# Kernel optimization log

Hardware: AMD Instinct MI355X
Metric: run time of the kernel (lower is better)

Reference implementation:

```python
import jax, jax.numpy as jnp
import numpy as np

B, D, L, H = 2048, 64, 64, 512  # batch, in_dim, latent_space, hidden


def setup_inputs() -> dict:
    key = jax.random.key(0)
    ks = jax.random.split(key, 12)
    inp = {
        "x": jax.random.normal(ks[0], (B, D), jnp.float32),
        "koopman": jax.random.normal(ks[1], (B, L, D), jnp.float32),
    }
    dims = [(L, H), (H, H), (H, H), (H, D)]
    k = 2
    for pfx in ("s", "t"):
        for j, (fi, fo) in enumerate(dims):
            inp[f"{pfx}W{j+1}"] = jax.random.normal(ks[k], (fi, fo), jnp.float32) / np.sqrt(fi).astype(np.float32)
            inp[f"{pfx}b{j+1}"] = jnp.zeros((fo,), jnp.float32)
            k += 1
    return inp


def _mlp(z, W1, b1, W2, b2, W3, b3, W4, b4):
    h = jnp.tanh(z @ W1 + b1)
    h = jnp.tanh(h @ W2 + b2)
    h = jnp.tanh(h @ W3 + b3)
    return h @ W4 + b4


def reference(x, koopman,
              sW1, sb1, sW2, sb2, sW3, sb3, sW4, sb4,
              tW1, tb1, tW2, tb2, tW3, tb3, tW4, tb4):
    # koopman: (B, L, D) -> z: (B, D, L); column i of the torch loop is z[:, i, :]
    z = jnp.swapaxes(koopman, 1, 2)
    s = _mlp(z, sW1, sb1, sW2, sb2, sW3, sb3, sW4, sb4)  # (B, D, D)
    t = _mlp(z, tW1, tb1, tW2, tb2, tW3, tb3, tW4, tb4)  # (B, D, D)
    # loop kept only output column i for input column i -> diagonal over last two dims
    ds = jnp.diagonal(s, axis1=1, axis2=2)  # (B, D)
    dt = jnp.diagonal(t, axis1=1, axis2=2)  # (B, D)
    return (x - dt) * jnp.exp(-ds)
```

## Files before the change

### kernel.cpp

```cpp
#include <hip/hip_runtime.h>


typedef _Float16 f16;
typedef _Float16 f16x8 __attribute__((ext_vector_type(8)));
typedef float f32x4 __attribute__((ext_vector_type(4)));

#define WPACK_PER_NET 589824
#define OFF_W1 0
#define OFF_W2 32768
#define OFF_W3 294912
#define OFF_W4T 557056
#define WPACK_BYTES (2u * WPACK_PER_NET * sizeof(f16))

__global__ void pack_weights(const float* __restrict__ sW1, const float* __restrict__ sW2,
                             const float* __restrict__ sW3, const float* __restrict__ sW4,
                             const float* __restrict__ tW1, const float* __restrict__ tW2,
                             const float* __restrict__ tW3, const float* __restrict__ tW4,
                             f16* __restrict__ dst) {
  int idx8 = (blockIdx.x * 256 + threadIdx.x) * 8;
  if (idx8 >= 2 * WPACK_PER_NET) return;
  int net = idx8 >= WPACK_PER_NET;
  int f = idx8 - net * WPACK_PER_NET;
  const float* W1 = net ? tW1 : sW1;
  const float* W2 = net ? tW2 : sW2;
  const float* W3 = net ? tW3 : sW3;
  const float* W4 = net ? tW4 : sW4;
  f16x8 o;
  if (f < OFF_W2) {
    int lane = (f >> 3) & 63, nt = (f >> 9) & 31, kk = f >> 14;
    int r0 = kk * 32 + (lane >> 4) * 8, c = nt * 16 + (lane & 15);
#pragma unroll
    for (int j = 0; j < 8; j++) o[j] = (f16)W1[(r0 + j) * 512 + c];
  } else if (f < OFF_W3) {
    int f2 = f - OFF_W2;
    int lane = (f2 >> 3) & 63, nt = (f2 >> 9) & 31, kk = f2 >> 14;
    int r0 = kk * 32 + (lane >> 4) * 8, c = nt * 16 + (lane & 15);
#pragma unroll
    for (int j = 0; j < 8; j++) o[j] = (f16)W2[(r0 + j) * 512 + c];
  } else if (f < OFF_W4T) {
    int f3 = f - OFF_W3;
    int lane = (f3 >> 3) & 63, nt = (f3 >> 9) & 31, kk = f3 >> 14;
    int r0 = kk * 32 + (lane >> 4) * 8, c = nt * 16 + (lane & 15);
#pragma unroll
    for (int j = 0; j < 8; j++) o[j] = (f16)W3[(r0 + j) * 512 + c];
  } else {
    int f4 = f - OFF_W4T;
    int i = f4 >> 9, k0 = f4 & 511;
#pragma unroll
    for (int j = 0; j < 8; j++) o[j] = (f16)W4[(k0 + j) * 64 + i];
  }
  *(f16x8*)(dst + net * WPACK_PER_NET + f) = o;
}

__device__ __forceinline__ int aidx(int m, int k) {
  return (((k >> 5) * 4 + (m >> 4)) * 64 + (m & 15) + ((k >> 3) & 3) * 16) * 8 + (k & 7);
}

__device__ __forceinline__ float fast_tanh(float x) {
  float e = __expf(x + x);
  return fmaf(-2.0f, __builtin_amdgcn_rcpf(e + 1.0f), 1.0f);
}

template <bool PACKED>
__device__ __forceinline__ void load_b(const f16* __restrict__ Wblk,
                                       const float* __restrict__ Wraw,
                                       int kk, int wave, int lane, f16x8* bdst) {
  if (PACKED) {
#pragma unroll
    for (int nt = 0; nt < 2; nt++)
      bdst[nt] = *(const f16x8*)(Wblk + kk * 16384 + ((wave * 2 + nt) * 64 + lane) * 8);
  } else {
    int n0 = wave * 32 + (lane & 15);
    int kb = kk * 32 + (lane >> 4) * 8;
#pragma unroll
    for (int nt = 0; nt < 2; nt++) {
      f16x8 v;
#pragma unroll
      for (int j = 0; j < 8; j++) v[j] = (f16)Wraw[(kb + j) * 512 + n0 + nt * 16];
      bdst[nt] = v;
    }
  }
}

template <int NS, bool PACKED>
__device__ __forceinline__ void mlp_layer(const f16* __restrict__ Wblk,
                                          const float* __restrict__ Wraw,
                                          const float* __restrict__ bias,
                                          const f16* Asrc, f16* Hout,
                                          int wave, int lane, int sbase) {
  f32x4 acc[4][2];
#pragma unroll
  for (int nt = 0; nt < 2; nt++) {
    float bv = bias[wave * 32 + nt * 16 + (lane & 15)];
#pragma unroll
    for (int mt = 0; mt < 4; mt++) acc[mt][nt] = f32x4{bv, bv, bv, bv};
  }

  f16x8 bb[2][2];
  load_b<PACKED>(Wblk, Wraw, 0, wave, lane, bb[0]);
#pragma unroll
  for (int kk = 0; kk < NS; kk++) {
    if (kk + 1 < NS) load_b<PACKED>(Wblk, Wraw, kk + 1, wave, lane, bb[(kk + 1) & 1]);
    const f16* ab = Asrc + kk * 2048 + lane * 8;
    f16x8 a[4];
#pragma unroll
    for (int mt = 0; mt < 4; mt++) a[mt] = *(const f16x8*)(ab + mt * 512);
#pragma unroll
    for (int mt = 0; mt < 4; mt++)
#pragma unroll
      for (int nt = 0; nt < 2; nt++)
        acc[mt][nt] = __builtin_amdgcn_mfma_f32_16x16x32_f16(a[mt], bb[kk & 1][nt],
                                                             acc[mt][nt], 0, 0, 0);
  }
  __syncthreads();

  f16* hb = Hout + sbase;
#pragma unroll
  for (int mt = 0; mt < 4; mt++)
#pragma unroll
    for (int nt = 0; nt < 2; nt++)
#pragma unroll
      for (int r = 0; r < 4; r++)
        hb[mt * 512 + nt * 256 + r * 8] = (f16)fast_tanh(acc[mt][nt][r]);
  __syncthreads();
}

template <bool PACKED>
__global__ __launch_bounds__(1024, 4) void decoder_main(
    const float* __restrict__ x, const float* __restrict__ koop,
    const f16* __restrict__ wpack,
    const float* __restrict__ sW1, const float* __restrict__ sW2,
    const float* __restrict__ sW3, const float* __restrict__ sW4,
    const float* __restrict__ tW1, const float* __restrict__ tW2,
    const float* __restrict__ tW3, const float* __restrict__ tW4,
    const float* __restrict__ sb1, const float* __restrict__ sb2,
    const float* __restrict__ sb3, const float* __restrict__ sb4,
    const float* __restrict__ tb1, const float* __restrict__ tb2,
    const float* __restrict__ tb3, const float* __restrict__ tb4,
    float* __restrict__ out) {
  __shared__ __align__(16) f16 ZA[4096];
  __shared__ __align__(16) f16 HA[32768];
  __shared__ float redBuf[2][64];

  const int b = blockIdx.x;
  const int t = threadIdx.x;
  const int wave = t >> 6, lane = t & 63;
  const int sbase =
      wave * 2048 + (lane >> 4) * 32 + ((lane & 15) >> 3) * 128 + (lane & 7);

  const float* kb = koop + b * 4096;
#pragma unroll
  for (int i = 0; i < 4; i++) {
    int flat = t + 1024 * i;
    ZA[aidx(flat & 63, flat >> 6)] = (f16)kb[flat];
  }
  __syncthreads();

  for (int net = 0; net < 2; net++) {
    const f16* wb = PACKED ? (wpack + net * WPACK_PER_NET) : (const f16*)0;
    const float* W1 = net ? tW1 : sW1;
    const float* W2 = net ? tW2 : sW2;
    const float* W3 = net ? tW3 : sW3;
    const float* W4 = net ? tW4 : sW4;
    const float* b1 = net ? tb1 : sb1;
    const float* b2 = net ? tb2 : sb2;
    const float* b3 = net ? tb3 : sb3;
    const float* b4 = net ? tb4 : sb4;
    mlp_layer<2, PACKED>(PACKED ? wb + OFF_W1 : 0, W1, b1, ZA, HA, wave, lane, sbase);
    mlp_layer<16, PACKED>(PACKED ? wb + OFF_W2 : 0, W2, b2, HA, HA, wave, lane, sbase);
    mlp_layer<16, PACKED>(PACKED ? wb + OFF_W3 : 0, W3, b3, HA, HA, wave, lane, sbase);

    int i = t >> 4, sub = t & 15;
    float p = 0.f;
#pragma unroll
    for (int q = 0; q < 4; q++) {
      int k0 = sub * 32 + q * 8;
      f16x8 hv = *(const f16x8*)&HA[aidx(i, k0)];
      if (PACKED) {
        f16x8 wv = *(const f16x8*)&wb[OFF_W4T + i * 512 + k0];
#pragma unroll
        for (int j = 0; j < 8; j++) p += (float)hv[j] * (float)wv[j];
      } else {
#pragma unroll
        for (int j = 0; j < 8; j++) p += (float)hv[j] * W4[(k0 + j) * 64 + i];
      }
    }
    p += __shfl_down(p, 8, 16);
    p += __shfl_down(p, 4, 16);
    p += __shfl_down(p, 2, 16);
    p += __shfl_down(p, 1, 16);
    if (sub == 0) redBuf[net][i] = p + b4[i];
    __syncthreads();
  }

  if (t < 64) {
    out[b * 64 + t] = (x[b * 64 + t] - redBuf[1][t]) * __expf(-redBuf[0][t]);
  }
}

extern "C" void kernel_launch(void* const* d_in, const int* in_sizes, int n_in,
                              void* d_out, int out_size, void* d_ws, size_t ws_size,
                              hipStream_t stream) {
  const float* x    = (const float*)d_in[0];
  const float* koop = (const float*)d_in[1];
  const float* sW1 = (const float*)d_in[2];  const float* sb1 = (const float*)d_in[3];
  const float* sW2 = (const float*)d_in[4];  const float* sb2 = (const float*)d_in[5];
  const float* sW3 = (const float*)d_in[6];  const float* sb3 = (const float*)d_in[7];
  const float* sW4 = (const float*)d_in[8];  const float* sb4 = (const float*)d_in[9];
  const float* tW1 = (const float*)d_in[10]; const float* tb1 = (const float*)d_in[11];
  const float* tW2 = (const float*)d_in[12]; const float* tb2 = (const float*)d_in[13];
  const float* tW3 = (const float*)d_in[14]; const float* tb3 = (const float*)d_in[15];
  const float* tW4 = (const float*)d_in[16]; const float* tb4 = (const float*)d_in[17];
  float* out = (float*)d_out;

  if (ws_size >= (size_t)WPACK_BYTES) {
    f16* wpack = (f16*)d_ws;
    pack_weights<<<576, 256, 0, stream>>>(sW1, sW2, sW3, sW4, tW1, tW2, tW3, tW4, wpack);
    decoder_main<true><<<2048, 1024, 0, stream>>>(
        x, koop, wpack, sW1, sW2, sW3, sW4, tW1, tW2, tW3, tW4,
        sb1, sb2, sb3, sb4, tb1, tb2, tb3, tb4, out);
  } else {
    decoder_main<false><<<2048, 1024, 0, stream>>>(
        x, koop, (const f16*)0, sW1, sW2, sW3, sW4, tW1, tW2, tW3, tW4,
        sb1, sb2, sb3, sb4, tb1, tb2, tb3, tb4, out);
  }
}
```

Before: 436.3 us.

## Split each batch row across two 512-thread blocks with wider per-wave N tiles

Each block now handles 32 of the 64 latent columns for one batch row, launching twice as many blocks with half the threads and half the shared memory. Waves compute a 2x4 MFMA tile (64 output columns) instead of 4x2, so fewer A fragments are reused across more B loads. Tanh is evaluated into registers before the barrier so it overlaps other waves. The cost is that every block streams the full weight set, doubling total weight reads from L2.

Result: slower. 494.7 us (+13.4%).

```diff
diff --git a/kernel.cpp b/kernel.cpp
--- a/kernel.cpp
+++ b/kernel.cpp
@@ -52,8 +52,8 @@
   *(f16x8*)(dst + net * WPACK_PER_NET + f) = o;
 }
 
-__device__ __forceinline__ int aidx(int m, int k) {
-  return (((k >> 5) * 4 + (m >> 4)) * 64 + (m & 15) + ((k >> 3) & 3) * 16) * 8 + (k & 7);
+__device__ __forceinline__ int aidx32(int m, int k) {
+  return (((k >> 5) * 2 + (m >> 4)) * 64 + (m & 15) + ((k >> 3) & 3) * 16) * 8 + (k & 7);
 }
 
 __device__ __forceinline__ float fast_tanh(float x) {
@@ -67,13 +67,13 @@
                                        int kk, int wave, int lane, f16x8* bdst) {
   if (PACKED) {
 #pragma unroll
-    for (int nt = 0; nt < 2; nt++)
-      bdst[nt] = *(const f16x8*)(Wblk + kk * 16384 + ((wave * 2 + nt) * 64 + lane) * 8);
+    for (int nt = 0; nt < 4; nt++)
+      bdst[nt] = *(const f16x8*)(Wblk + kk * 16384 + ((wave * 4 + nt) * 64 + lane) * 8);
   } else {
-    int n0 = wave * 32 + (lane & 15);
+    int n0 = wave * 64 + (lane & 15);
     int kb = kk * 32 + (lane >> 4) * 8;
 #pragma unroll
-    for (int nt = 0; nt < 2; nt++) {
+    for (int nt = 0; nt < 4; nt++) {
       f16x8 v;
 #pragma unroll
       for (int j = 0; j < 8; j++) v[j] = (f16)Wraw[(kb + j) * 512 + n0 + nt * 16];
@@ -88,45 +88,56 @@
                                           const float* __restrict__ bias,
                                           const f16* Asrc, f16* Hout,
                                           int wave, int lane, int sbase) {
-  f32x4 acc[4][2];
-#pragma unroll
-  for (int nt = 0; nt < 2; nt++) {
-    float bv = bias[wave * 32 + nt * 16 + (lane & 15)];
-#pragma unroll
-    for (int mt = 0; mt < 4; mt++) acc[mt][nt] = f32x4{bv, bv, bv, bv};
-  }
-
-  f16x8 bb[2][2];
+  f32x4 acc[2][4];
+#pragma unroll
+  for (int nt = 0; nt < 4; nt++) {
+    float bv = bias[wave * 64 + nt * 16 + (lane & 15)];
+#pragma unroll
+    for (int mt = 0; mt < 2; mt++) acc[mt][nt] = f32x4{bv, bv, bv, bv};
+  }
+
+  f16x8 bb[2][4];
   load_b<PACKED>(Wblk, Wraw, 0, wave, lane, bb[0]);
 #pragma unroll
   for (int kk = 0; kk < NS; kk++) {
     if (kk + 1 < NS) load_b<PACKED>(Wblk, Wraw, kk + 1, wave, lane, bb[(kk + 1) & 1]);
-    const f16* ab = Asrc + kk * 2048 + lane * 8;
-    f16x8 a[4];
-#pragma unroll
-    for (int mt = 0; mt < 4; mt++) a[mt] = *(const f16x8*)(ab + mt * 512);
-#pragma unroll
-    for (int mt = 0; mt < 4; mt++)
-#pragma unroll
-      for (int nt = 0; nt < 2; nt++)
+    const f16* ab = Asrc + kk * 1024 + lane * 8;
+    f16x8 a[2];
+#pragma unroll
+    for (int mt = 0; mt < 2; mt++) a[mt] = *(const f16x8*)(ab + mt * 512);
+#pragma unroll
+    for (int mt = 0; mt < 2; mt++)
+#pragma unroll
+      for (int nt = 0; nt < 4; nt++)
         acc[mt][nt] = __builtin_amdgcn_mfma_f32_16x16x32_f16(a[mt], bb[kk & 1][nt],
                                                              acc[mt][nt], 0, 0, 0);
   }
+
+  f16 hreg[32];
+#pragma unroll
+  for (int mt = 0; mt < 2; mt++)
+#pragma unroll
+    for (int nt = 0; nt < 4; nt++)
+#pragma unroll
+      for (int r = 0; r < 4; r++)
+        hreg[(mt * 4 + nt) * 4 + r] = (f16)fast_tanh(acc[mt][nt][r]);
+
   __syncthreads();
 
   f16* hb = Hout + sbase;
 #pragma unroll
-  for (int mt = 0; mt < 4; mt++)
-#pragma unroll
-    for (int nt = 0; nt < 2; nt++)
+  for (int mt = 0; mt < 2; mt++)
+#pragma unroll
+    for (int nt = 0; nt < 4; nt++)
 #pragma unroll
       for (int r = 0; r < 4; r++)
-        hb[mt * 512 + nt * 256 + r * 8] = (f16)fast_tanh(acc[mt][nt][r]);
+        hb[(nt >> 1) * 1024 + (nt & 1) * 256 + mt * 512 + r * 8] =
+            hreg[(mt * 4 + nt) * 4 + r];
   __syncthreads();
 }
 
 template <bool PACKED>
-__global__ __launch_bounds__(1024, 4) void decoder_main(
+__global__ __launch_bounds__(512, 4) void decoder_main(
     const float* __restrict__ x, const float* __restrict__ koop,
     const f16* __restrict__ wpack,
     const float* __restrict__ sW1, const float* __restrict__ sW2,
@@ -138,21 +149,23 @@
     const float* __restrict__ tb1, const float* __restrict__ tb2,
     const float* __restrict__ tb3, const float* __restrict__ tb4,
     float* __restrict__ out) {
-  __shared__ __align__(16) f16 ZA[4096];
-  __shared__ __align__(16) f16 HA[32768];
-  __shared__ float redBuf[2][64];
-
-  const int b = blockIdx.x;
+  __shared__ __align__(16) f16 ZA[2048];
+  __shared__ __align__(16) f16 HA[16384];
+  __shared__ float redBuf[2][32];
+
+  const int bid = blockIdx.x;
+  const int b = bid >> 1, rr = bid & 1;
   const int t = threadIdx.x;
   const int wave = t >> 6, lane = t & 63;
   const int sbase =
       wave * 2048 + (lane >> 4) * 32 + ((lane & 15) >> 3) * 128 + (lane & 7);
 
-  const float* kb = koop + b * 4096;
+  const float* kb = koop + b * 4096 + rr * 32;
 #pragma unroll
   for (int i = 0; i < 4; i++) {
-    int flat = t + 1024 * i;
-    ZA[aidx(flat & 63, flat >> 6)] = (f16)kb[flat];
+    int flat = t + 512 * i;
+    int l = flat >> 5, dl = flat & 31;
+    ZA[aidx32(dl, l)] = (f16)kb[l * 64 + dl];
   }
   __syncthreads();
 
@@ -171,30 +184,32 @@
     mlp_layer<16, PACKED>(PACKED ? wb + OFF_W3 : 0, W3, b3, HA, HA, wave, lane, sbase);
 
     int i = t >> 4, sub = t & 15;
+    int ig = rr * 32 + i;
     float p = 0.f;
 #pragma unroll
     for (int q = 0; q < 4; q++) {
       int k0 = sub * 32 + q * 8;
-      f16x8 hv = *(const f16x8*)&HA[aidx(i, k0)];
+      f16x8 hv = *(const f16x8*)&HA[aidx32(i, k0)];
       if (PACKED) {
-        f16x8 wv = *(const f16x8*)&wb[OFF_W4T + i * 512 + k0];
+        f16x8 wv = *(const f16x8*)&wb[OFF_W4T + ig * 512 + k0];
 #pragma unroll
         for (int j = 0; j < 8; j++) p += (float)hv[j] * (float)wv[j];
       } else {
 #pragma unroll
-        for (int j = 0; j < 8; j++) p += (float)hv[j] * W4[(k0 + j) * 64 + i];
+        for (int j = 0; j < 8; j++) p += (float)hv[j] * W4[(k0 + j) * 64 + ig];
       }
     }
     p += __shfl_down(p, 8, 16);
     p += __shfl_down(p, 4, 16);
     p += __shfl_down(p, 2, 16);
     p += __shfl_down(p, 1, 16);
-    if (sub == 0) redBuf[net][i] = p + b4[i];
+    if (sub == 0) redBuf[net][i] = p + b4[ig];
     __syncthreads();
   }
 
-  if (t < 64) {
-    out[b * 64 + t] = (x[b * 64 + t] - redBuf[1][t]) * __expf(-redBuf[0][t]);
+  if (t < 32) {
+    int ig = rr * 32 + t;
+    out[b * 64 + ig] = (x[b * 64 + ig] - redBuf[1][t]) * __expf(-redBuf[0][t]);
   }
 }
 
@@ -216,11 +231,11 @@
   if (ws_size >= (size_t)WPACK_BYTES) {
     f16* wpack = (f16*)d_ws;
     pack_weights<<<576, 256, 0, stream>>>(sW1, sW2, sW3, sW4, tW1, tW2, tW3, tW4, wpack);
-    decoder_main<true><<<2048, 1024, 0, stream>>>(
+    decoder_main<true><<<4096, 512, 0, stream>>>(
         x, koop, wpack, sW1, sW2, sW3, sW4, tW1, tW2, tW3, tW4,
         sb1, sb2, sb3, sb4, tb1, tb2, tb3, tb4, out);
   } else {
-    decoder_main<false><<<2048, 1024, 0, stream>>>(
+    decoder_main<false><<<4096, 512, 0, stream>>>(
         x, koop, (const f16*)0, sW1, sW2, sW3, sW4, tW1, tW2, tW3, tW4,
         sb1, sb2, sb3, sb4, tb1, tb2, tb3, tb4, out);
   }
```

## Halve block to 512 threads with two column passes and cross-layer weight prefetch

Applied to the files above, without the earlier changes.

Each block now runs 8 waves instead of 16, and each wave computes two 256-column halves per layer in sequence. The tanh results are held in registers until a single barrier-protected write to shared memory. The first weight fragment of the next pass, the next layer, or the next network is prefetched during the last k-step, which hides load latency across layer boundaries. The final W4 dot product is remapped to 8 threads per output. The aim is to cut barrier cost and raise work per wave, but it adds register pressure from hreg, and there are fewer waves to hide latency.

New measurement: 476.2 us. +9.1%, slower.

```diff
diff --git a/kernel.cpp b/kernel.cpp
--- a/kernel.cpp
+++ b/kernel.cpp
@@ -64,13 +64,15 @@
 template <bool PACKED>
 __device__ __forceinline__ void load_b(const f16* __restrict__ Wblk,
                                        const float* __restrict__ Wraw,
-                                       int kk, int wave, int lane, f16x8* bdst) {
+                                       int kk, int pass, int wave, int lane,
+                                       f16x8* bdst) {
   if (PACKED) {
 #pragma unroll
     for (int nt = 0; nt < 2; nt++)
-      bdst[nt] = *(const f16x8*)(Wblk + kk * 16384 + ((wave * 2 + nt) * 64 + lane) * 8);
+      bdst[nt] = *(const f16x8*)(Wblk + kk * 16384 +
+                                 ((pass * 16 + wave * 2 + nt) * 64 + lane) * 8);
   } else {
-    int n0 = wave * 32 + (lane & 15);
+    int n0 = pass * 256 + wave * 32 + (lane & 15);
     int kb = kk * 32 + (lane >> 4) * 8;
 #pragma unroll
     for (int nt = 0; nt < 2; nt++) {
@@ -87,46 +89,69 @@
                                           const float* __restrict__ Wraw,
                                           const float* __restrict__ bias,
                                           const f16* Asrc, f16* Hout,
-                                          int wave, int lane, int sbase) {
-  f32x4 acc[4][2];
-#pragma unroll
-  for (int nt = 0; nt < 2; nt++) {
-    float bv = bias[wave * 32 + nt * 16 + (lane & 15)];
-#pragma unroll
-    for (int mt = 0; mt < 4; mt++) acc[mt][nt] = f32x4{bv, bv, bv, bv};
-  }
-
-  f16x8 bb[2][2];
-  load_b<PACKED>(Wblk, Wraw, 0, wave, lane, bb[0]);
-#pragma unroll
-  for (int kk = 0; kk < NS; kk++) {
-    if (kk + 1 < NS) load_b<PACKED>(Wblk, Wraw, kk + 1, wave, lane, bb[(kk + 1) & 1]);
-    const f16* ab = Asrc + kk * 2048 + lane * 8;
-    f16x8 a[4];
-#pragma unroll
-    for (int mt = 0; mt < 4; mt++) a[mt] = *(const f16x8*)(ab + mt * 512);
+                                          int wave, int lane, int sbase,
+                                          f16x8* pb,
+                                          const f16* __restrict__ WblkN,
+                                          const float* __restrict__ WrawN,
+                                          bool hasNext) {
+  f16 hreg[2][32];
+#pragma unroll
+  for (int pass = 0; pass < 2; pass++) {
+    f32x4 acc[4][2];
+#pragma unroll
+    for (int nt = 0; nt < 2; nt++) {
+      float bv = bias[pass * 256 + wave * 32 + nt * 16 + (lane & 15)];
+#pragma unroll
+      for (int mt = 0; mt < 4; mt++) acc[mt][nt] = f32x4{bv, bv, bv, bv};
+    }
+    f16x8 bb[2][2];
+    bb[0][0] = pb[0];
+    bb[0][1] = pb[1];
+#pragma unroll
+    for (int kk = 0; kk < NS; kk++) {
+      if (kk + 1 < NS) {
+        load_b<PACKED>(Wblk, Wraw, kk + 1, pass, wave, lane, bb[(kk + 1) & 1]);
+      } else if (pass == 0) {
+        load_b<PACKED>(Wblk, Wraw, 0, 1, wave, lane, pb);
+      } else if (hasNext) {
+        load_b<PACKED>(WblkN, WrawN, 0, 0, wave, lane, pb);
+      }
+      const f16* ab = Asrc + kk * 2048 + lane * 8;
+#pragma unroll
+      for (int mt = 0; mt < 4; mt++) {
+        f16x8 a = *(const f16x8*)(ab + mt * 512);
+#pragma unroll
+        for (int nt = 0; nt < 2; nt++)
+          acc[mt][nt] = __builtin_amdgcn_mfma_f32_16x16x32_f16(a, bb[kk & 1][nt],
+                                                               acc[mt][nt], 0, 0, 0);
+      }
+    }
 #pragma unroll
     for (int mt = 0; mt < 4; mt++)
 #pragma unroll
       for (int nt = 0; nt < 2; nt++)
-        acc[mt][nt] = __builtin_amdgcn_mfma_f32_16x16x32_f16(a[mt], bb[kk & 1][nt],
-                                                             acc[mt][nt], 0, 0, 0);
+#pragma unroll
+        for (int r = 0; r < 4; r++)
+          hreg[pass][(mt * 2 + nt) * 4 + r] = (f16)fast_tanh(acc[mt][nt][r]);
   }
   __syncthreads();
 
   f16* hb = Hout + sbase;
 #pragma unroll
-  for (int mt = 0; mt < 4; mt++)
-#pragma unroll
-    for (int nt = 0; nt < 2; nt++)
-#pragma unroll
-      for (int r = 0; r < 4; r++)
-        hb[mt * 512 + nt * 256 + r * 8] = (f16)fast_tanh(acc[mt][nt][r]);
+  for (int pass = 0; pass < 2; pass++)
+#pragma unroll
+    for (int mt = 0; mt < 4; mt++)
+#pragma unroll
+      for (int nt = 0; nt < 2; nt++)
+#pragma unroll
+        for (int r = 0; r < 4; r++)
+          hb[pass * 16384 + mt * 512 + nt * 256 + r * 8] =
+              hreg[pass][(mt * 2 + nt) * 4 + r];
   __syncthreads();
 }
 
 template <bool PACKED>
-__global__ __launch_bounds__(1024, 4) void decoder_main(
+__global__ __launch_bounds__(512, 4) void decoder_main(
     const float* __restrict__ x, const float* __restrict__ koop,
     const f16* __restrict__ wpack,
     const float* __restrict__ sW1, const float* __restrict__ sW2,
@@ -150,10 +175,12 @@
 
   const float* kb = koop + b * 4096;
 #pragma unroll
-  for (int i = 0; i < 4; i++) {
-    int flat = t + 1024 * i;
+  for (int i = 0; i < 8; i++) {
+    int flat = t + 512 * i;
     ZA[aidx(flat & 63, flat >> 6)] = (f16)kb[flat];
   }
+  f16x8 pb[2];
+  load_b<PACKED>(PACKED ? wpack + OFF_W1 : 0, sW1, 0, 0, wave, lane, pb);
   __syncthreads();
 
   for (int net = 0; net < 2; net++) {
@@ -166,15 +193,19 @@
     const float* b2 = net ? tb2 : sb2;
     const float* b3 = net ? tb3 : sb3;
     const float* b4 = net ? tb4 : sb4;
-    mlp_layer<2, PACKED>(PACKED ? wb + OFF_W1 : 0, W1, b1, ZA, HA, wave, lane, sbase);
-    mlp_layer<16, PACKED>(PACKED ? wb + OFF_W2 : 0, W2, b2, HA, HA, wave, lane, sbase);
-    mlp_layer<16, PACKED>(PACKED ? wb + OFF_W3 : 0, W3, b3, HA, HA, wave, lane, sbase);
-
-    int i = t >> 4, sub = t & 15;
+    mlp_layer<2, PACKED>(PACKED ? wb + OFF_W1 : 0, W1, b1, ZA, HA, wave, lane, sbase,
+                         pb, PACKED ? wb + OFF_W2 : 0, W2, true);
+    mlp_layer<16, PACKED>(PACKED ? wb + OFF_W2 : 0, W2, b2, HA, HA, wave, lane, sbase,
+                          pb, PACKED ? wb + OFF_W3 : 0, W3, true);
+    mlp_layer<16, PACKED>(PACKED ? wb + OFF_W3 : 0, W3, b3, HA, HA, wave, lane, sbase,
+                          pb, (net == 0 && PACKED) ? wpack + WPACK_PER_NET + OFF_W1 : 0,
+                          net == 0 ? tW1 : 0, net == 0);
+
+    int i = t >> 3, sub = t & 7;
     float p = 0.f;
 #pragma unroll
-    for (int q = 0; q < 4; q++) {
-      int k0 = sub * 32 + q * 8;
+    for (int q = 0; q < 8; q++) {
+      int k0 = sub * 64 + q * 8;
       f16x8 hv = *(const f16x8*)&HA[aidx(i, k0)];
       if (PACKED) {
         f16x8 wv = *(const f16x8*)&wb[OFF_W4T + i * 512 + k0];
@@ -185,10 +216,9 @@
         for (int j = 0; j < 8; j++) p += (float)hv[j] * W4[(k0 + j) * 64 + i];
       }
     }
-    p += __shfl_down(p, 8, 16);
-    p += __shfl_down(p, 4, 16);
-    p += __shfl_down(p, 2, 16);
-    p += __shfl_down(p, 1, 16);
+    p += __shfl_down(p, 4, 8);
+    p += __shfl_down(p, 2, 8);
+    p += __shfl_down(p, 1, 8);
     if (sub == 0) redBuf[net][i] = p + b4[i];
     __syncthreads();
   }
@@ -216,11 +246,11 @@
   if (ws_size >= (size_t)WPACK_BYTES) {
     f16* wpack = (f16*)d_ws;
     pack_weights<<<576, 256, 0, stream>>>(sW1, sW2, sW3, sW4, tW1, tW2, tW3, tW4, wpack);
-    decoder_main<true><<<2048, 1024, 0, stream>>>(
+    decoder_main<true><<<2048, 512, 0, stream>>>(
         x, koop, wpack, sW1, sW2, sW3, sW4, tW1, tW2, tW3, tW4,
         sb1, sb2, sb3, sb4, tb1, tb2, tb3, tb4, out);
   } else {
-    decoder_main<false><<<2048, 1024, 0, stream>>>(
+    decoder_main<false><<<2048, 512, 0, stream>>>(
         x, koop, (const f16*)0, sW1, sW2, sW3, sW4, tW1, tW2, tW3, tW4,
         sb1, sb2, sb3, sb4, tb1, tb2, tb3, tb4, out);
   }
```

## Switch MLP layers to 32x32x16 MFMA with 512-thread blocks

Applied to the files above, without the earlier changes.

Replaces the 16x16x32 MFMA tiling with 32x32x16 MFMA. Each of 8 waves now computes a 64x64 output tile instead of 16 waves computing 64x32, and the weight-packing and LDS activation layouts are reworked to match. Each block loads less B-operand data per output element and issues fewer MFMA instructions. The pre-epilogue barrier is dropped for the first layer, whose input and output buffers differ. The costs are more accumulator registers per thread, fewer threads per block, and a new LDS store pattern that may cause bank conflicts.

Result: slower. 455.5 us (+4.4%).

```diff
diff --git a/kernel.cpp b/kernel.cpp
--- a/kernel.cpp
+++ b/kernel.cpp
@@ -3,7 +3,7 @@
 
 typedef _Float16 f16;
 typedef _Float16 f16x8 __attribute__((ext_vector_type(8)));
-typedef float f32x4 __attribute__((ext_vector_type(4)));
+typedef float f32x16 __attribute__((ext_vector_type(16)));
 
 #define WPACK_PER_NET 589824
 #define OFF_W1 0
@@ -27,20 +27,20 @@
   const float* W4 = net ? tW4 : sW4;
   f16x8 o;
   if (f < OFF_W2) {
-    int lane = (f >> 3) & 63, nt = (f >> 9) & 31, kk = f >> 14;
-    int r0 = kk * 32 + (lane >> 4) * 8, c = nt * 16 + (lane & 15);
+    int lane = (f >> 3) & 63, ctg = (f >> 9) & 15, ks = f >> 13;
+    int r0 = ks * 16 + (lane >> 5) * 8, c = ctg * 32 + (lane & 31);
 #pragma unroll
     for (int j = 0; j < 8; j++) o[j] = (f16)W1[(r0 + j) * 512 + c];
   } else if (f < OFF_W3) {
     int f2 = f - OFF_W2;
-    int lane = (f2 >> 3) & 63, nt = (f2 >> 9) & 31, kk = f2 >> 14;
-    int r0 = kk * 32 + (lane >> 4) * 8, c = nt * 16 + (lane & 15);
+    int lane = (f2 >> 3) & 63, ctg = (f2 >> 9) & 15, ks = f2 >> 13;
+    int r0 = ks * 16 + (lane >> 5) * 8, c = ctg * 32 + (lane & 31);
 #pragma unroll
     for (int j = 0; j < 8; j++) o[j] = (f16)W2[(r0 + j) * 512 + c];
   } else if (f < OFF_W4T) {
     int f3 = f - OFF_W3;
-    int lane = (f3 >> 3) & 63, nt = (f3 >> 9) & 31, kk = f3 >> 14;
-    int r0 = kk * 32 + (lane >> 4) * 8, c = nt * 16 + (lane & 15);
+    int lane = (f3 >> 3) & 63, ctg = (f3 >> 9) & 15, ks = f3 >> 13;
+    int r0 = ks * 16 + (lane >> 5) * 8, c = ctg * 32 + (lane & 31);
 #pragma unroll
     for (int j = 0; j < 8; j++) o[j] = (f16)W3[(r0 + j) * 512 + c];
   } else {
@@ -53,7 +53,7 @@
 }
 
 __device__ __forceinline__ int aidx(int m, int k) {
-  return (((k >> 5) * 4 + (m >> 4)) * 64 + (m & 15) + ((k >> 3) & 3) * 16) * 8 + (k & 7);
+  return ((k >> 4) * 2 + (m >> 5)) * 512 + ((m & 31) + 32 * ((k >> 3) & 1)) * 8 + (k & 7);
 }
 
 __device__ __forceinline__ float fast_tanh(float x) {
@@ -64,69 +64,72 @@
 template <bool PACKED>
 __device__ __forceinline__ void load_b(const f16* __restrict__ Wblk,
                                        const float* __restrict__ Wraw,
-                                       int kk, int wave, int lane, f16x8* bdst) {
+                                       int ks, int wave, int lane, f16x8* bdst) {
   if (PACKED) {
 #pragma unroll
-    for (int nt = 0; nt < 2; nt++)
-      bdst[nt] = *(const f16x8*)(Wblk + kk * 16384 + ((wave * 2 + nt) * 64 + lane) * 8);
+    for (int ct = 0; ct < 2; ct++)
+      bdst[ct] = *(const f16x8*)(Wblk + ((ks * 16 + wave * 2 + ct) * 64 + lane) * 8);
   } else {
-    int n0 = wave * 32 + (lane & 15);
-    int kb = kk * 32 + (lane >> 4) * 8;
-#pragma unroll
-    for (int nt = 0; nt < 2; nt++) {
+    int r0 = ks * 16 + (lane >> 5) * 8;
+    int n0 = wave * 64 + (lane & 31);
+#pragma unroll
+    for (int ct = 0; ct < 2; ct++) {
       f16x8 v;
 #pragma unroll
-      for (int j = 0; j < 8; j++) v[j] = (f16)Wraw[(kb + j) * 512 + n0 + nt * 16];
-      bdst[nt] = v;
+      for (int j = 0; j < 8; j++) v[j] = (f16)Wraw[(r0 + j) * 512 + n0 + ct * 32];
+      bdst[ct] = v;
     }
   }
 }
 
-template <int NS, bool PACKED>
+template <int NS, bool PACKED, bool ALIASED>
 __device__ __forceinline__ void mlp_layer(const f16* __restrict__ Wblk,
                                           const float* __restrict__ Wraw,
                                           const float* __restrict__ bias,
                                           const f16* Asrc, f16* Hout,
                                           int wave, int lane, int sbase) {
-  f32x4 acc[4][2];
-#pragma unroll
-  for (int nt = 0; nt < 2; nt++) {
-    float bv = bias[wave * 32 + nt * 16 + (lane & 15)];
-#pragma unroll
-    for (int mt = 0; mt < 4; mt++) acc[mt][nt] = f32x4{bv, bv, bv, bv};
+  f32x16 acc[2][2];
+#pragma unroll
+  for (int ct = 0; ct < 2; ct++) {
+    float bv = bias[wave * 64 + ct * 32 + (lane & 31)];
+#pragma unroll
+    for (int mt = 0; mt < 2; mt++)
+#pragma unroll
+      for (int e = 0; e < 16; e++) acc[mt][ct][e] = bv;
   }
 
   f16x8 bb[2][2];
   load_b<PACKED>(Wblk, Wraw, 0, wave, lane, bb[0]);
 #pragma unroll
-  for (int kk = 0; kk < NS; kk++) {
-    if (kk + 1 < NS) load_b<PACKED>(Wblk, Wraw, kk + 1, wave, lane, bb[(kk + 1) & 1]);
-    const f16* ab = Asrc + kk * 2048 + lane * 8;
-    f16x8 a[4];
-#pragma unroll
-    for (int mt = 0; mt < 4; mt++) a[mt] = *(const f16x8*)(ab + mt * 512);
-#pragma unroll
-    for (int mt = 0; mt < 4; mt++)
-#pragma unroll
-      for (int nt = 0; nt < 2; nt++)
-        acc[mt][nt] = __builtin_amdgcn_mfma_f32_16x16x32_f16(a[mt], bb[kk & 1][nt],
-                                                             acc[mt][nt], 0, 0, 0);
-  }
+  for (int ks = 0; ks < NS; ks++) {
+    if (ks + 1 < NS) load_b<PACKED>(Wblk, Wraw, ks + 1, wave, lane, bb[(ks + 1) & 1]);
+    const f16* ab = Asrc + ks * 1024 + lane * 8;
+    f16x8 a0 = *(const f16x8*)ab;
+    f16x8 a1 = *(const f16x8*)(ab + 512);
+#pragma unroll
+    for (int ct = 0; ct < 2; ct++) {
+      acc[0][ct] = __builtin_amdgcn_mfma_f32_32x32x16_f16(a0, bb[ks & 1][ct],
+                                                          acc[0][ct], 0, 0, 0);
+      acc[1][ct] = __builtin_amdgcn_mfma_f32_32x32x16_f16(a1, bb[ks & 1][ct],
+                                                          acc[1][ct], 0, 0, 0);
+    }
+  }
+  if (ALIASED) __syncthreads();
+
+  f16* hb = Hout + sbase;
+#pragma unroll
+  for (int mt = 0; mt < 2; mt++)
+#pragma unroll
+    for (int ct = 0; ct < 2; ct++)
+#pragma unroll
+      for (int reg = 0; reg < 16; reg++)
+        hb[ct * 2048 + mt * 512 + (reg >> 2) * 64 + (reg & 3) * 8] =
+            (f16)fast_tanh(acc[mt][ct][reg]);
   __syncthreads();
-
-  f16* hb = Hout + sbase;
-#pragma unroll
-  for (int mt = 0; mt < 4; mt++)
-#pragma unroll
-    for (int nt = 0; nt < 2; nt++)
-#pragma unroll
-      for (int r = 0; r < 4; r++)
-        hb[mt * 512 + nt * 256 + r * 8] = (f16)fast_tanh(acc[mt][nt][r]);
-  __syncthreads();
 }
 
 template <bool PACKED>
-__global__ __launch_bounds__(1024, 4) void decoder_main(
+__global__ __launch_bounds__(512, 4) void decoder_main(
     const float* __restrict__ x, const float* __restrict__ koop,
     const f16* __restrict__ wpack,
     const float* __restrict__ sW1, const float* __restrict__ sW2,
@@ -145,13 +148,13 @@
   const int b = blockIdx.x;
   const int t = threadIdx.x;
   const int wave = t >> 6, lane = t & 63;
-  const int sbase =
-      wave * 2048 + (lane >> 4) * 32 + ((lane & 15) >> 3) * 128 + (lane & 7);
+  const int sbase = wave * 4096 + ((lane >> 4) & 1) * 1024 +
+                    ((lane >> 3) & 1) * 256 + (lane >> 5) * 32 + (lane & 7);
 
   const float* kb = koop + b * 4096;
 #pragma unroll
-  for (int i = 0; i < 4; i++) {
-    int flat = t + 1024 * i;
+  for (int i = 0; i < 8; i++) {
+    int flat = t + 512 * i;
     ZA[aidx(flat & 63, flat >> 6)] = (f16)kb[flat];
   }
   __syncthreads();
@@ -166,15 +169,18 @@
     const float* b2 = net ? tb2 : sb2;
     const float* b3 = net ? tb3 : sb3;
     const float* b4 = net ? tb4 : sb4;
-    mlp_layer<2, PACKED>(PACKED ? wb + OFF_W1 : 0, W1, b1, ZA, HA, wave, lane, sbase);
-    mlp_layer<16, PACKED>(PACKED ? wb + OFF_W2 : 0, W2, b2, HA, HA, wave, lane, sbase);
-    mlp_layer<16, PACKED>(PACKED ? wb + OFF_W3 : 0, W3, b3, HA, HA, wave, lane, sbase);
-
-    int i = t >> 4, sub = t & 15;
+    mlp_layer<4, PACKED, false>(PACKED ? wb + OFF_W1 : 0, W1, b1, ZA, HA,
+                                wave, lane, sbase);
+    mlp_layer<32, PACKED, true>(PACKED ? wb + OFF_W2 : 0, W2, b2, HA, HA,
+                                wave, lane, sbase);
+    mlp_layer<32, PACKED, true>(PACKED ? wb + OFF_W3 : 0, W3, b3, HA, HA,
+                                wave, lane, sbase);
+
+    int i = t >> 3, sub = t & 7;
     float p = 0.f;
 #pragma unroll
-    for (int q = 0; q < 4; q++) {
-      int k0 = sub * 32 + q * 8;
+    for (int q = 0; q < 8; q++) {
+      int k0 = sub * 64 + q * 8;
       f16x8 hv = *(const f16x8*)&HA[aidx(i, k0)];
       if (PACKED) {
         f16x8 wv = *(const f16x8*)&wb[OFF_W4T + i * 512 + k0];
@@ -185,10 +191,9 @@
         for (int j = 0; j < 8; j++) p += (float)hv[j] * W4[(k0 + j) * 64 + i];
       }
     }
-    p += __shfl_down(p, 8, 16);
-    p += __shfl_down(p, 4, 16);
-    p += __shfl_down(p, 2, 16);
-    p += __shfl_down(p, 1, 16);
+    p += __shfl_down(p, 4, 8);
+    p += __shfl_down(p, 2, 8);
+    p += __shfl_down(p, 1, 8);
     if (sub == 0) redBuf[net][i] = p + b4[i];
     __syncthreads();
   }
@@ -216,11 +221,11 @@
   if (ws_size >= (size_t)WPACK_BYTES) {
     f16* wpack = (f16*)d_ws;
     pack_weights<<<576, 256, 0, stream>>>(sW1, sW2, sW3, sW4, tW1, tW2, tW3, tW4, wpack);
-    decoder_main<true><<<2048, 1024, 0, stream>>>(
+    decoder_main<true><<<2048, 512, 0, stream>>>(
         x, koop, wpack, sW1, sW2, sW3, sW4, tW1, tW2, tW3, tW4,
         sb1, sb2, sb3, sb4, tb1, tb2, tb3, tb4, out);
   } else {
-    decoder_main<false><<<2048, 1024, 0, stream>>>(
+    decoder_main<false><<<2048, 512, 0, stream>>>(
         x, koop, (const f16*)0, sW1, sW2, sW3, sW4, tW1, tW2, tW3, tW4,
         sb1, sb2, sb3, sb4, tb1, tb2, tb3, tb4, out);
   }
```
